# Optimization experiments

Hardware: AMD Instinct MI355X
Metric: run time of the kernel (lower is better)

## Reference

```python
import jax, jax.numpy as jnp
import numpy as np

N, DV, M, DC = 1024, 4, 512, 8
E = N * DV  # 4096 edges; N*DV == M*DC
EPS32 = jnp.float32(1.1920929e-07)  # torch.finfo(torch.float32).eps


def _build_masks():
    rng = np.random.default_rng(0)
    var_of_edge = np.repeat(np.arange(N), DV)                # edge -> variable node
    chk_of_edge = rng.permutation(np.repeat(np.arange(M), DC))  # edge -> check node
    eye = np.eye(E, dtype=bool)
    w_in_to_odd = np.zeros((N, E), dtype=np.float32)
    w_in_to_odd[var_of_edge, np.arange(E)] = 1.0
    same_var = var_of_edge[:, None] == var_of_edge[None, :]
    same_chk = chk_of_edge[:, None] == chk_of_edge[None, :]
    w_even_to_odd = (same_var & ~eye).astype(np.float32)     # extrinsic var-node connectivity
    w_odd_to_even = (same_chk & ~eye).astype(np.float32)     # extrinsic check-node connectivity
    w_even_to_out = np.zeros((E, N), dtype=np.float32)
    w_even_to_out[np.arange(E), var_of_edge] = 1.0
    return w_in_to_odd, w_odd_to_even, w_even_to_odd, w_even_to_out


def setup_inputs() -> dict:
    key = jax.random.key(0)
    w_in_to_odd, w_odd_to_even, w_even_to_odd, w_even_to_out = _build_masks()
    x = 2.0 * jax.random.normal(key, (N, 1), dtype=jnp.float32)  # channel LLRs
    return {
        "x": x,
        "w_in_to_odd": jnp.asarray(w_in_to_odd),
        "w_odd_to_even": jnp.asarray(w_odd_to_even),
        "w_even_to_odd": jnp.asarray(w_even_to_odd),
        "w_even_to_out": jnp.asarray(w_even_to_out),
    }


def _activation_even(odd, w_odd_to_even):
    # odd: [E,1]; repeat across columns then mask -> aux[i,j] = w[i,j]*odd[i]
    aux = w_odd_to_even * odd                      # [E,E]
    aux = jnp.where(aux == 0.0, 1.0, aux)          # zeros (non-edges) -> multiplicative identity
    v = jnp.prod(aux, axis=0)                      # [E] product over incoming messages
    v = jnp.where(v >= 1.0, 1.0 - EPS32, v)
    v = jnp.where(v <= -1.0, -1.0 + EPS32, v)
    return (2.0 * jnp.arctanh(v))[:, None]         # [E,1]


def reference(x, w_in_to_odd, w_odd_to_even, w_even_to_odd, w_even_to_out):
    llr_part = w_in_to_odd.T @ x                   # [E,1], reused every odd layer
    # layer 1: even input is zeros (first_even_layer_output / first_w_even_to_odd)
    odd = jnp.tanh(0.5 * llr_part)
    even = _activation_even(odd, w_odd_to_even)
    for _ in range(4):                             # iterations 2..5 (shared 'rnn'/'spa' weights)
        odd = jnp.tanh(0.5 * (llr_part + w_even_to_odd.T @ even))
        even = _activation_even(odd, w_odd_to_even)
    out = x + w_even_to_out.T @ even               # [N,1]
    return jax.nn.sigmoid(out)
```

## Files before the change

kernel.cpp:

```cpp
#include <hip/hip_runtime.h>


#define En 4096
#define Nn 1024
#define Mn 512
#define EPSF 1.1920929e-07f
#define MAGIC 0x7E57A11F
#define NSOLVE 16
#define CPB (Mn / NSOLVE)
#define VPB (Nn / NSOLVE)

__device__ __forceinline__ int ldi_b(const int* p) {
  return __hip_atomic_load(p, __ATOMIC_RELAXED, __HIP_MEMORY_SCOPE_AGENT);
}
__device__ __forceinline__ float ldf_b(const float* p) {
  return __hip_atomic_load(p, __ATOMIC_RELAXED, __HIP_MEMORY_SCOPE_AGENT);
}
__device__ __forceinline__ void sti_b(int* p, int v) {
  __hip_atomic_store(p, v, __ATOMIC_RELAXED, __HIP_MEMORY_SCOPE_AGENT);
}
__device__ __forceinline__ void stf_b(float* p, float v) {
  __hip_atomic_store(p, v, __ATOMIC_RELAXED, __HIP_MEMORY_SCOPE_AGENT);
}

__device__ __forceinline__ void gbar(int* arrive, int bar, int t, int b) {
  __syncthreads();
  if (t == 0) sti_b(&arrive[bar * NSOLVE + b], MAGIC);
  if (t < NSOLVE) {
    while (ldi_b(&arrive[bar * NSOLVE + t]) != MAGIC)
      __builtin_amdgcn_s_sleep(1);
  }
  __syncthreads();
}

__global__ __launch_bounds__(1024) void spa_fused(
    const float* __restrict__ w, const float* __restrict__ x,
    float* __restrict__ out, int* __restrict__ f_g,
    int* __restrict__ sflag, float* __restrict__ evs_g,
    int* __restrict__ arrive) {
  __shared__ int   fs[En];
  __shared__ int   slotmap[En];
  __shared__ int   ce[En];
  __shared__ int   cnt[Mn];
  __shared__ int   wtot[16];
  __shared__ float xch[256];

  const int t    = threadIdx.x;
  const int lane = t & 63;
  const int wv   = t >> 6;
  const int b    = blockIdx.x;

  {
    const int row = b * 16 + wv;
    const float4* rowp = (const float4*)(w + (size_t)row * En);
    float4 v0 = rowp[lane];
    float4 v1 = rowp[64 + lane];
    float4 v2 = rowp[128 + lane];
    float4 v3 = rowp[192 + lane];
    for (int base = 0;; base += 256) {
      bool any = (v0.x != 0.0f) | (v0.y != 0.0f) | (v0.z != 0.0f) | (v0.w != 0.0f);
      unsigned long long m = __ballot(any);
      if (m) {
        if (lane == __ffsll(m) - 1) {
          int off = (v0.x != 0.0f) ? 0 : (v0.y != 0.0f) ? 1 : (v0.z != 0.0f) ? 2 : 3;
          sti_b(&f_g[row], base + 4 * lane + off);
        }
        break;
      }
      v0 = v1; v1 = v2; v2 = v3;
      int nxt = base + 1024;
      if (nxt > En - 256) nxt = En - 256;
      v3 = rowp[(nxt >> 2) + lane];
    }
  }
  __syncthreads();
  if (t == 0) sti_b(&sflag[b], MAGIC);
  if (b >= NSOLVE) return;

  if (t < Mn) cnt[t] = 0;

  if (t < 256) {
    while (ldi_b(&sflag[t]) != MAGIC) __builtin_amdgcn_s_sleep(2);
  }
  __syncthreads();

  int4 fv;
  fv.x = ldi_b(&f_g[4 * t + 0]);
  fv.y = ldi_b(&f_g[4 * t + 1]);
  fv.z = ldi_b(&f_g[4 * t + 2]);
  fv.w = ldi_b(&f_g[4 * t + 3]);
  *((int4*)&fs[4 * t]) = fv;
  __syncthreads();

  const int fearr[4] = {fv.x, fv.y, fv.z, fv.w};
  int  keys[4];
  bool ismin[4];
#pragma unroll
  for (int k = 0; k < 4; ++k) {
    int e   = 4 * t + k;
    int fe  = fearr[k];
    int ffe = fs[fe];
    keys[k]  = (ffe == e && e < fe) ? e : fe;
    ismin[k] = (keys[k] == e);
  }
  const unsigned long long ltmask = (1ull << lane) - 1ull;
  int pre = 0;
  int rank[4];
#pragma unroll
  for (int k = 0; k < 4; ++k) {
    unsigned long long bb = __ballot(ismin[k]);
    rank[k] = pre + (int)__popcll(bb & ltmask);
    pre    += (int)__popcll(bb);
  }
  if (lane == 0) wtot[wv] = pre;
  __syncthreads();
  int wbase = 0;
  for (int w2 = 0; w2 < wv; ++w2) wbase += wtot[w2];
#pragma unroll
  for (int k = 0; k < 4; ++k)
    if (ismin[k]) slotmap[4 * t + k] = wbase + rank[k];
  __syncthreads();

#pragma unroll
  for (int k = 0; k < 4; ++k) {
    int c = slotmap[keys[k]];
    int p = atomicAdd(&cnt[c], 1);
    ce[c * 8 + p] = 4 * t + k;
  }
  __syncthreads();

  if (t < Mn) {
    int4 a = *((int4*)&ce[t * 8]);
    int4 bq = *((int4*)&ce[t * 8 + 4]);
    int s0 = a.x, s1 = a.y, s2 = a.z, s3 = a.w;
    int s4 = bq.x, s5 = bq.y, s6 = bq.z, s7 = bq.w;
#define CEX(p, q) { int lo_ = min(p, q), hi_ = max(p, q); p = lo_; q = hi_; }
    CEX(s0, s1); CEX(s2, s3); CEX(s0, s2); CEX(s1, s3); CEX(s1, s2);
    CEX(s4, s5); CEX(s6, s7); CEX(s4, s6); CEX(s5, s7); CEX(s5, s6);
    CEX(s0, s4); CEX(s2, s6); CEX(s1, s5); CEX(s3, s7);
    CEX(s2, s4); CEX(s3, s5);
    CEX(s1, s2); CEX(s3, s4); CEX(s5, s6);
#undef CEX
    *((int4*)&ce[t * 8])     = make_int4(s0, s1, s2, s3);
    *((int4*)&ce[t * 8 + 4]) = make_int4(s4, s5, s6, s7);
  }
  __syncthreads();

  int   e = 0, kv = 0, vhome = 0;
  float xv = 0.0f, od = 0.0f;
  if (t < 256) {
    e     = ce[b * 256 + t];
    vhome = e >> 2;
    kv    = e & 3;
    xv    = x[vhome];
    od    = tanhf(0.5f * xv);
  }

  for (int it = 0; it < 5; ++it) {
    if (t < 256) xch[t] = (od == 0.0f) ? 1.0f : od;
    __syncthreads();
    if (t < 256) {
      int gb = t & ~7;
      int ek = t & 7;
      int j0 = (ek == 0) ? 1 : 0;
      float p = xch[gb + j0];
      for (int j = j0 + 1; j < 8; ++j)
        if (j != ek) p *= xch[gb + j];
      if (p >= 1.0f)       p =  1.0f - EPSF;
      else if (p <= -1.0f) p = -1.0f + EPSF;
      stf_b(&evs_g[e], 2.0f * atanhf(p));
    }
    gbar(arrive, it, t, b);

    if (it < 4) {
      if (t < 256) {
        float s = 0.0f;
        for (int j = 0; j < 4; ++j)
          if (j != kv) s += ldf_b(&evs_g[4 * vhome + j]);
        od = tanhf(0.5f * (xv + s));
      }
    }
  }

  if (t < VPB) {
    int v = b * VPB + t;
    float e0 = ldf_b(&evs_g[4 * v + 0]);
    float e1 = ldf_b(&evs_g[4 * v + 1]);
    float e2 = ldf_b(&evs_g[4 * v + 2]);
    float e3 = ldf_b(&evs_g[4 * v + 3]);
    float s4 = ((e0 + e1) + e2) + e3;
    float z  = x[v] + s4;
    out[v]   = 1.0f / (1.0f + expf(-z));
  }
}

extern "C" void kernel_launch(void* const* d_in, const int* in_sizes, int n_in,
                              void* d_out, int out_size, void* d_ws,
                              size_t ws_size, hipStream_t stream) {
  const float* x    = (const float*)d_in[0];
  const float* w_oe = (const float*)d_in[2];
  float* out = (float*)d_out;

  int*   f      = (int*)d_ws;
  int*   sflag  = f + En;
  float* evs_g  = (float*)(sflag + 256);
  int*   arrive = (int*)(evs_g + En);

  spa_fused<<<dim3(256), dim3(1024), 0, stream>>>(w_oe, x, out, f, sflag,
                                                  evs_g, arrive);
}
```

Before: 164.1 us.

## Replace global barriers with per-value tagged 64-bit messages and wave shuffles

Every message value is packed with a magic tag into a 64-bit word. Consumers spin only on the specific values they need, which replaces the per-block ready flags and the all-block global barrier each iteration. Check-node products now use wave shuffles instead of a shared-memory exchange plus __syncthreads. Per-iteration buffers avoid reuse races. Risks: tags are never cleared between launches, so stale workspace could pass the readiness check. Spins are bounded by PBOUND and fall through silently.

```diff
diff --git a/kernel.cpp b/kernel.cpp
--- a/kernel.cpp
+++ b/kernel.cpp
@@ -5,45 +5,35 @@
 #define Nn 1024
 #define Mn 512
 #define EPSF 1.1920929e-07f
-#define MAGIC 0x7E57A11F
+#define MAGICI 0x7E57A11F
 #define NSOLVE 16
 #define CPB (Mn / NSOLVE)
 #define VPB (Nn / NSOLVE)
-
-__device__ __forceinline__ int ldi_b(const int* p) {
+#define PBOUND (1 << 18)
+
+typedef unsigned long long u64;
+
+__device__ __forceinline__ u64 ldq_b(const u64* p) {
   return __hip_atomic_load(p, __ATOMIC_RELAXED, __HIP_MEMORY_SCOPE_AGENT);
 }
-__device__ __forceinline__ float ldf_b(const float* p) {
-  return __hip_atomic_load(p, __ATOMIC_RELAXED, __HIP_MEMORY_SCOPE_AGENT);
-}
-__device__ __forceinline__ void sti_b(int* p, int v) {
+__device__ __forceinline__ void stq_b(u64* p, u64 v) {
   __hip_atomic_store(p, v, __ATOMIC_RELAXED, __HIP_MEMORY_SCOPE_AGENT);
 }
-__device__ __forceinline__ void stf_b(float* p, float v) {
-  __hip_atomic_store(p, v, __ATOMIC_RELAXED, __HIP_MEMORY_SCOPE_AGENT);
-}
-
-__device__ __forceinline__ void gbar(int* arrive, int bar, int t, int b) {
-  __syncthreads();
-  if (t == 0) sti_b(&arrive[bar * NSOLVE + b], MAGIC);
-  if (t < NSOLVE) {
-    while (ldi_b(&arrive[bar * NSOLVE + t]) != MAGIC)
-      __builtin_amdgcn_s_sleep(1);
-  }
-  __syncthreads();
-}
+__device__ __forceinline__ u64 packf(float f) {
+  return ((u64)MAGICI << 32) | (u64)__float_as_uint(f);
+}
+__device__ __forceinline__ bool tagged(u64 v) { return (v >> 32) == (u64)MAGICI; }
+__device__ __forceinline__ float payload(u64 v) { return __uint_as_float((unsigned)v); }
 
 __global__ __launch_bounds__(1024) void spa_fused(
     const float* __restrict__ w, const float* __restrict__ x,
-    float* __restrict__ out, int* __restrict__ f_g,
-    int* __restrict__ sflag, float* __restrict__ evs_g,
-    int* __restrict__ arrive) {
-  __shared__ int   fs[En];
-  __shared__ int   slotmap[En];
-  __shared__ int   ce[En];
-  __shared__ int   cnt[Mn];
-  __shared__ int   wtot[16];
-  __shared__ float xch[256];
+    float* __restrict__ out, u64* __restrict__ fq,
+    u64* __restrict__ evq) {
+  __shared__ int fs[En];
+  __shared__ int slotmap[En];
+  __shared__ int ce[En];
+  __shared__ int cnt[Mn];
+  __shared__ int wtot[16];
 
   const int t    = threadIdx.x;
   const int lane = t & 63;
@@ -63,7 +53,7 @@
       if (m) {
         if (lane == __ffsll(m) - 1) {
           int off = (v0.x != 0.0f) ? 0 : (v0.y != 0.0f) ? 1 : (v0.z != 0.0f) ? 2 : 3;
-          sti_b(&f_g[row], base + 4 * lane + off);
+          stq_b(&fq[row], ((u64)MAGICI << 32) | (u64)(unsigned)(base + 4 * lane + off));
         }
         break;
       }
@@ -73,26 +63,29 @@
       v3 = rowp[(nxt >> 2) + lane];
     }
   }
-  __syncthreads();
-  if (t == 0) sti_b(&sflag[b], MAGIC);
   if (b >= NSOLVE) return;
 
   if (t < Mn) cnt[t] = 0;
 
-  if (t < 256) {
-    while (ldi_b(&sflag[t]) != MAGIC) __builtin_amdgcn_s_sleep(2);
-  }
-  __syncthreads();
-
-  int4 fv;
-  fv.x = ldi_b(&f_g[4 * t + 0]);
-  fv.y = ldi_b(&f_g[4 * t + 1]);
-  fv.z = ldi_b(&f_g[4 * t + 2]);
-  fv.w = ldi_b(&f_g[4 * t + 3]);
-  *((int4*)&fs[4 * t]) = fv;
-  __syncthreads();
-
-  const int fearr[4] = {fv.x, fv.y, fv.z, fv.w};
+  u64 q0, q1, q2, q3;
+  {
+    int gd = 0;
+    do {
+      q0 = ldq_b(&fq[4 * t + 0]);
+      q1 = ldq_b(&fq[4 * t + 1]);
+      q2 = ldq_b(&fq[4 * t + 2]);
+      q3 = ldq_b(&fq[4 * t + 3]);
+    } while (!(tagged(q0) && tagged(q1) && tagged(q2) && tagged(q3)) &&
+             ++gd < PBOUND);
+  }
+  fs[4 * t + 0] = (int)(unsigned)q0;
+  fs[4 * t + 1] = (int)(unsigned)q1;
+  fs[4 * t + 2] = (int)(unsigned)q2;
+  fs[4 * t + 3] = (int)(unsigned)q3;
+  __syncthreads();
+
+  const int fearr[4] = {(int)(unsigned)q0, (int)(unsigned)q1,
+                        (int)(unsigned)q2, (int)(unsigned)q3};
   int  keys[4];
   bool ismin[4];
 #pragma unroll
@@ -146,37 +139,50 @@
   }
   __syncthreads();
 
-  int   e = 0, kv = 0, vhome = 0;
+  int   e = 0, ek = 0, kv = 0, vhome = 0, ja = 0, jb = 0, jc = 0;
   float xv = 0.0f, od = 0.0f;
   if (t < 256) {
     e     = ce[b * 256 + t];
+    ek    = t & 7;
     vhome = e >> 2;
     kv    = e & 3;
+    ja    = (kv == 0) ? 1 : 0;
+    jb    = (kv <= 1) ? 2 : 1;
+    jc    = (kv == 3) ? 2 : 3;
     xv    = x[vhome];
     od    = tanhf(0.5f * xv);
   }
+  const int gb8 = lane & ~7;
 
   for (int it = 0; it < 5; ++it) {
-    if (t < 256) xch[t] = (od == 0.0f) ? 1.0f : od;
-    __syncthreads();
     if (t < 256) {
-      int gb = t & ~7;
-      int ek = t & 7;
+      float fk = (od == 0.0f) ? 1.0f : od;
+      float f0 = __shfl(fk, gb8 + 0), f1 = __shfl(fk, gb8 + 1);
+      float f2 = __shfl(fk, gb8 + 2), f3 = __shfl(fk, gb8 + 3);
+      float f4 = __shfl(fk, gb8 + 4), f5 = __shfl(fk, gb8 + 5);
+      float f6 = __shfl(fk, gb8 + 6), f7 = __shfl(fk, gb8 + 7);
+      const float fa[8] = {f0, f1, f2, f3, f4, f5, f6, f7};
       int j0 = (ek == 0) ? 1 : 0;
-      float p = xch[gb + j0];
-      for (int j = j0 + 1; j < 8; ++j)
-        if (j != ek) p *= xch[gb + j];
+      float p = fa[j0];
+#pragma unroll
+      for (int j = 1; j < 8; ++j)
+        p *= ((j > j0) && (j != ek)) ? fa[j] : 1.0f;
       if (p >= 1.0f)       p =  1.0f - EPSF;
       else if (p <= -1.0f) p = -1.0f + EPSF;
-      stf_b(&evs_g[e], 2.0f * atanhf(p));
-    }
-    gbar(arrive, it, t, b);
-
-    if (it < 4) {
-      if (t < 256) {
+      stq_b(&evq[it * En + e], packf(2.0f * atanhf(p)));
+
+      if (it < 4) {
+        u64 a0, a1, a2;
+        int gd = 0;
+        do {
+          a0 = ldq_b(&evq[it * En + 4 * vhome + ja]);
+          a1 = ldq_b(&evq[it * En + 4 * vhome + jb]);
+          a2 = ldq_b(&evq[it * En + 4 * vhome + jc]);
+        } while (!(tagged(a0) && tagged(a1) && tagged(a2)) && ++gd < PBOUND);
         float s = 0.0f;
-        for (int j = 0; j < 4; ++j)
-          if (j != kv) s += ldf_b(&evs_g[4 * vhome + j]);
+        s += payload(a0);
+        s += payload(a1);
+        s += payload(a2);
         od = tanhf(0.5f * (xv + s));
       }
     }
@@ -184,11 +190,16 @@
 
   if (t < VPB) {
     int v = b * VPB + t;
-    float e0 = ldf_b(&evs_g[4 * v + 0]);
-    float e1 = ldf_b(&evs_g[4 * v + 1]);
-    float e2 = ldf_b(&evs_g[4 * v + 2]);
-    float e3 = ldf_b(&evs_g[4 * v + 3]);
-    float s4 = ((e0 + e1) + e2) + e3;
+    u64 a0, a1, a2, a3;
+    int gd = 0;
+    do {
+      a0 = ldq_b(&evq[4 * En + 4 * v + 0]);
+      a1 = ldq_b(&evq[4 * En + 4 * v + 1]);
+      a2 = ldq_b(&evq[4 * En + 4 * v + 2]);
+      a3 = ldq_b(&evq[4 * En + 4 * v + 3]);
+    } while (!(tagged(a0) && tagged(a1) && tagged(a2) && tagged(a3)) &&
+             ++gd < PBOUND);
+    float s4 = ((payload(a0) + payload(a1)) + payload(a2)) + payload(a3);
     float z  = x[v] + s4;
     out[v]   = 1.0f / (1.0f + expf(-z));
   }
@@ -201,11 +212,8 @@
   const float* w_oe = (const float*)d_in[2];
   float* out = (float*)d_out;
 
-  int*   f      = (int*)d_ws;
-  int*   sflag  = f + En;
-  float* evs_g  = (float*)(sflag + 256);
-  int*   arrive = (int*)(evs_g + En);
-
-  spa_fused<<<dim3(256), dim3(1024), 0, stream>>>(w_oe, x, out, f, sflag,
-                                                  evs_g, arrive);
-}
+  u64* fq  = (u64*)d_ws;
+  u64* evq = fq + En;
+
+  spa_fused<<<dim3(256), dim3(1024), 0, stream>>>(w_oe, x, out, fq, evq);
+}
```

Result: slower. 169.1 us (+3.0%).
